# Kernel tuning notes

Hardware: AMD Instinct MI355X
Metric: run time of the kernel (lower is better)

The kernel has to match this reference:

```python
import jax, jax.numpy as jnp
import numpy as np

N_NODES = 50000
N_EDGES = 800000
IN_DIM = 128
HID_DIM = 128
N_CLASSES = 64


def gcn_conv(x, edge_index, W, b):
    """PyG GCNConv: add self-loops, sym deg^-1/2 norm, xW, scatter-add, +bias."""
    n = x.shape[0]
    loop = jnp.arange(n, dtype=edge_index.dtype)
    src = jnp.concatenate([edge_index[0], loop])  # [E+N]
    dst = jnp.concatenate([edge_index[1], loop])  # [E+N]
    ones = jnp.ones(src.shape[0], dtype=x.dtype)
    deg = jax.ops.segment_sum(ones, dst, num_segments=n)  # in-degree incl self-loop
    dinv = jnp.where(deg > 0, jax.lax.rsqrt(deg), jnp.zeros_like(deg))
    norm = dinv[src] * dinv[dst]  # [E+N]
    h = x @ W  # [N, out]
    msg = h[src] * norm[:, None]  # [E+N, out] gather + scale
    out = jax.ops.segment_sum(msg, dst, num_segments=n)  # scatter-add
    return out + b


def setup_inputs() -> dict:
    key = jax.random.key(0)
    k1, k2, k3, k4, k5 = jax.random.split(key, 5)
    x = jax.random.normal(k1, (N_NODES, IN_DIM), dtype=jnp.float32)
    edge_index = jax.random.randint(k2, (2, N_EDGES), 0, N_NODES, dtype=jnp.int64)
    # Glorot-style init for the two GCNConv linear weights; zero biases (PyG default)
    s1 = 1.0 / np.sqrt(IN_DIM)
    s2 = 1.0 / np.sqrt(HID_DIM)
    W1 = jax.random.uniform(k3, (IN_DIM, HID_DIM), jnp.float32, -s1, s1)
    b1 = jnp.zeros((HID_DIM,), jnp.float32)
    W2 = jax.random.uniform(k4, (HID_DIM, N_CLASSES), jnp.float32, -s2, s2)
    b2 = jnp.zeros((N_CLASSES,), jnp.float32)
    return {"x": x, "edge_index": edge_index, "W1": W1, "b1": b1, "W2": W2, "b2": b2}


def reference(x, edge_index, W1, b1, W2, b2):
    h = gcn_conv(x, edge_index, W1, b1)
    h = jax.nn.relu(h)
    out = gcn_conv(h, edge_index, W2, b2)
    return out
```

## Files before the change

### kernel.cpp

```cpp
#include <hip/hip_runtime.h>
#include <hip/hip_bf16.h>
#include <hip/hip_fp16.h>


#define NODES_PER_BLOCK 4
#define CHUNK 4096
#define BCAP 8192

typedef unsigned int uint;
typedef _Float16 f16x8 __attribute__((ext_vector_type(8)));
typedef float f32x4 __attribute__((ext_vector_type(4)));

__device__ __forceinline__ float2 h2f(uint v) {
  __half2 h;
  __builtin_memcpy(&h, &v, 4);
  return __half22float2(h);
}

__device__ __forceinline__ uint f2h(float a, float b) {
  __half2 h = __halves2half2(__float2half_rn(a), __float2half_rn(b));
  uint r;
  __builtin_memcpy(&r, &h, 4);
  return r;
}

__global__ void detect64_k(const int* ei, int* flag) {
  int lane = threadIdx.x & 63;
  unsigned long long m = __ballot(ei[2 * lane + 1] != 0);
  if (threadIdx.x == 0) *flag = (m == 0ULL) ? 1 : 0;
}

__global__ __launch_bounds__(256) void hist_k(const int* __restrict__ ei,
                                              const int* __restrict__ flag,
                                              int* __restrict__ gh,
                                              int E, int nchunk, int nbuck) {
  __shared__ int h[256];
  int c = blockIdx.x;
  for (int i = threadIdx.x; i < 256; i += 256) h[i] = 0;
  __syncthreads();
  int is64 = *flag;
  int base = c * CHUNK;
  int lim = min(CHUNK, E - base);
  for (int i = threadIdx.x; i < lim; i += 256) {
    int e = base + i;
    int d = is64 ? ei[2 * ((size_t)E + e)] : ei[(size_t)E + e];
    atomicAdd(&h[d >> 8], 1);
  }
  __syncthreads();
  for (int k = threadIdx.x; k < nbuck; k += 256) gh[k * nchunk + c] = h[k];
}

__global__ __launch_bounds__(256) void tot_k(const int* __restrict__ gh,
                                             int* __restrict__ totals, int nchunk) {
  __shared__ int sd[256];
  int k = blockIdx.x;
  int s = 0;
  for (int i = threadIdx.x; i < nchunk; i += 256) s += gh[k * nchunk + i];
  sd[threadIdx.x] = s;
  __syncthreads();
  for (int o = 128; o > 0; o >>= 1) {
    if (threadIdx.x < o) sd[threadIdx.x] += sd[threadIdx.x + o];
    __syncthreads();
  }
  if (threadIdx.x == 0) totals[k] = sd[0];
}

__global__ __launch_bounds__(256) void scanrow_k(int* __restrict__ gh,
                                                 const int* __restrict__ totals,
                                                 int* __restrict__ bucketStart,
                                                 int* __restrict__ offsets,
                                                 int nchunk, int nbuck, int N, int E) {
  __shared__ int st[256];
  int k = blockIdx.x;
  int t = threadIdx.x;
  int v = (t < nbuck && t < k) ? totals[t] : 0;
  st[t] = v;
  __syncthreads();
  for (int o = 128; o > 0; o >>= 1) {
    if (t < o) st[t] += st[t + o];
    __syncthreads();
  }
  int bs = st[0];
  if (t == 0) {
    bucketStart[k] = bs;
    if (k == nbuck - 1) { bucketStart[nbuck] = E; offsets[N] = E; }
  }
  __syncthreads();
  int x = (t < nchunk) ? gh[k * nchunk + t] : 0;
  st[t] = x;
  __syncthreads();
  int incl = x;
  for (int o = 1; o < 256; o <<= 1) {
    int add = (t >= o) ? st[t - o] : 0;
    __syncthreads();
    incl += add;
    st[t] = incl;
    __syncthreads();
  }
  if (t < nchunk) gh[k * nchunk + t] = bs + (incl - x);
}

__global__ __launch_bounds__(256) void part_k(const int* __restrict__ ei,
                                              const int* __restrict__ flag,
                                              const int* __restrict__ gh,
                                              int* __restrict__ tmp,
                                              int E, int nchunk, int nbuck) {
  __shared__ int cur[256];
  int c = blockIdx.x;
  for (int i = threadIdx.x; i < nbuck; i += 256) cur[i] = gh[i * nchunk + c];
  __syncthreads();
  int is64 = *flag;
  int base = c * CHUNK;
  int lim = min(CHUNK, E - base);
  for (int i = threadIdx.x; i < lim; i += 256) {
    int e = base + i;
    int s, d;
    if (is64) {
      s = ei[2 * (size_t)e];
      d = ei[2 * ((size_t)E + e)];
    } else {
      s = ei[e];
      d = ei[(size_t)E + e];
    }
    int p = atomicAdd(&cur[d >> 8], 1);
    tmp[p] = s | ((d & 255) << 16);
  }
}

__global__ __launch_bounds__(256) void bucket_k(const int* __restrict__ tmp,
                                                const int* __restrict__ bucketStart,
                                                int* __restrict__ csr_src,
                                                int* __restrict__ offsets,
                                                float* __restrict__ dinv,
                                                int N) {
  __shared__ int ebuf[BCAP];
  __shared__ int cnt[256];
  __shared__ int st[256];
  __shared__ int lofs[256];
  int k = blockIdx.x;
  int b0 = bucketStart[k], b1 = bucketStart[k + 1];
  int sz = b1 - b0;
  int t = threadIdx.x;
  cnt[t] = 0;
  __syncthreads();
  bool inlds = (sz <= BCAP);
  if (inlds) {
    for (int i = t; i < sz; i += 256) {
      int v = tmp[b0 + i];
      ebuf[i] = v;
      atomicAdd(&cnt[v >> 16], 1);
    }
  } else {
    for (int i = t; i < sz; i += 256) atomicAdd(&cnt[tmp[b0 + i] >> 16], 1);
  }
  __syncthreads();
  int x = cnt[t];
  st[t] = x;
  __syncthreads();
  int incl = x;
  for (int o = 1; o < 256; o <<= 1) {
    int add = (t >= o) ? st[t - o] : 0;
    __syncthreads();
    incl += add;
    st[t] = incl;
    __syncthreads();
  }
  lofs[t] = incl - x;
  int node = k * 256 + t;
  if (node < N) {
    offsets[node] = b0 + lofs[t];
    dinv[node] = rsqrtf((float)(x + 1));
  }
  __syncthreads();
  cnt[t] = lofs[t];
  __syncthreads();
  if (inlds) {
    for (int i = t; i < sz; i += 256) {
      int v = ebuf[i];
      int p = atomicAdd(&cnt[v >> 16], 1);
      csr_src[b0 + p] = v & 0xFFFF;
    }
  } else {
    for (int i = t; i < sz; i += 256) {
      int v = tmp[b0 + i];
      int p = atomicAdd(&cnt[v >> 16], 1);
      csr_src[b0 + p] = v & 0xFFFF;
    }
  }
}

__global__ void prep_k(const float* __restrict__ W, _Float16* __restrict__ P,
                       int NC, int total) {
  int idx = blockIdx.x * blockDim.x + threadIdx.x;
  if (idx >= total) return;
  int NF = NC >> 4;
  int j = idx & 7;
  int l = (idx >> 3) & 63;
  int rest = idx >> 9;
  int c = rest % NF;
  int t = rest / NF;
  int k = t * 32 + ((l >> 4) << 3) + j;
  int col = c * 16 + (l & 15);
  P[idx] = (_Float16)W[(size_t)k * NC + col];
}

template <int NC, bool A16>
__global__ __launch_bounds__(256) void mfma_gemm_k(const void* __restrict__ Xv,
                                                   const _Float16* __restrict__ Wp,
                                                   const float* __restrict__ dinv,
                                                   _Float16* __restrict__ H, int M) {
  constexpr int NF = NC / 16;
  int lane = threadIdx.x & 63;
  int w = threadIdx.x >> 6;
  int row0 = blockIdx.x * 64 + w * 16;
  int arow = row0 + (lane & 15);
  bool av = arow < M;
  const uint4* wp = (const uint4*)Wp;

  f32x4 acc[NF];
#pragma unroll
  for (int c = 0; c < NF; ++c) acc[c] = (f32x4){0.f, 0.f, 0.f, 0.f};

#pragma unroll
  for (int t = 0; t < 4; ++t) {
    f16x8 a;
    if constexpr (A16) {
      const _Float16* xr = (const _Float16*)Xv + (size_t)arow * 128 + ((lane >> 4) << 3);
      uint4 araw = av ? *(const uint4*)(xr + t * 32)
                      : make_uint4(0u, 0u, 0u, 0u);
      __builtin_memcpy(&a, &araw, 16);
    } else {
      const float* xr = (const float*)Xv + (size_t)arow * 128 + ((lane >> 4) << 3);
      float4 lo = av ? *(const float4*)(xr + t * 32)
                     : make_float4(0.f, 0.f, 0.f, 0.f);
      float4 hi = av ? *(const float4*)(xr + t * 32 + 4)
                     : make_float4(0.f, 0.f, 0.f, 0.f);
      a[0] = (_Float16)lo.x; a[1] = (_Float16)lo.y;
      a[2] = (_Float16)lo.z; a[3] = (_Float16)lo.w;
      a[4] = (_Float16)hi.x; a[5] = (_Float16)hi.y;
      a[6] = (_Float16)hi.z; a[7] = (_Float16)hi.w;
    }
#pragma unroll
    for (int c = 0; c < NF; ++c) {
      uint4 braw = wp[(t * NF + c) * 64 + lane];
      f16x8 b;
      __builtin_memcpy(&b, &braw, 16);
      acc[c] = __builtin_amdgcn_mfma_f32_16x16x32_f16(a, b, acc[c], 0, 0, 0);
    }
  }

  int rbase = row0 + ((lane >> 4) << 2);
#pragma unroll
  for (int r = 0; r < 4; ++r) {
    int row = rbase + r;
    if (row < M) {
      float di = dinv[row];
#pragma unroll
      for (int c = 0; c < NF; ++c)
        H[(size_t)row * NC + c * 16 + (lane & 15)] = (_Float16)(di * acc[c][r]);
    }
  }
}

__global__ __launch_bounds__(256) void agg1_k(const uint* __restrict__ hp,
                                              const float* __restrict__ dinv,
                                              const int* __restrict__ offsets,
                                              const int* __restrict__ csr_src,
                                              const float* __restrict__ b,
                                              uint* __restrict__ y, int n) {
  int wave = threadIdx.x >> 6;
  int lane = threadIdx.x & 63;
  int node = blockIdx.x * NODES_PER_BLOCK + wave;
  if (node >= n) return;
  int beg = offsets[node], end = offsets[node + 1];
  int deg = end - beg;
  float2 self = h2f(hp[(size_t)node * 64 + lane]);
  float ax = self.x, ay = self.y;
  int sv = 0;
  if (lane < deg) sv = csr_src[beg + lane];
  int lim = deg < 64 ? deg : 64;
  int e = 0;
  for (; e + 8 <= lim; e += 8) {
    int s0 = __shfl(sv, e + 0), s1 = __shfl(sv, e + 1);
    int s2 = __shfl(sv, e + 2), s3 = __shfl(sv, e + 3);
    int s4 = __shfl(sv, e + 4), s5 = __shfl(sv, e + 5);
    int s6 = __shfl(sv, e + 6), s7 = __shfl(sv, e + 7);
    uint u0 = hp[(size_t)s0 * 64 + lane];
    uint u1 = hp[(size_t)s1 * 64 + lane];
    uint u2 = hp[(size_t)s2 * 64 + lane];
    uint u3 = hp[(size_t)s3 * 64 + lane];
    uint u4 = hp[(size_t)s4 * 64 + lane];
    uint u5 = hp[(size_t)s5 * 64 + lane];
    uint u6 = hp[(size_t)s6 * 64 + lane];
    uint u7 = hp[(size_t)s7 * 64 + lane];
    float2 v0 = h2f(u0), v1 = h2f(u1), v2 = h2f(u2), v3 = h2f(u3);
    float2 v4 = h2f(u4), v5 = h2f(u5), v6 = h2f(u6), v7 = h2f(u7);
    ax += ((v0.x + v1.x) + (v2.x + v3.x)) + ((v4.x + v5.x) + (v6.x + v7.x));
    ay += ((v0.y + v1.y) + (v2.y + v3.y)) + ((v4.y + v5.y) + (v6.y + v7.y));
  }
  for (; e < lim; ++e) {
    int s = __shfl(sv, e);
    float2 v = h2f(hp[(size_t)s * 64 + lane]);
    ax += v.x;
    ay += v.y;
  }
  for (int ee = beg + 64; ee < end; ++ee) {
    float2 v = h2f(hp[(size_t)csr_src[ee] * 64 + lane]);
    ax += v.x;
    ay += v.y;
  }
  float di = dinv[node];
  float2 bb = ((const float2*)b)[lane];
  float ox = fmaxf(fmaf(di, ax, bb.x), 0.0f);
  float oy = fmaxf(fmaf(di, ay, bb.y), 0.0f);
  y[(size_t)node * 64 + lane] = f2h(ox, oy);
}

__global__ __launch_bounds__(256) void agg2_k(const uint* __restrict__ hp,
                                              const float* __restrict__ dinv,
                                              const int* __restrict__ offsets,
                                              const int* __restrict__ csr_src,
                                              const float* __restrict__ b,
                                              float* __restrict__ out, int n) {
  int wv = threadIdx.x >> 6;
  int lane = threadIdx.x & 63;
  int half = lane >> 5;
  int fl = lane & 31;
  int node = blockIdx.x * 8 + wv * 2 + half;
  if (node >= n) return;
  int beg = offsets[node], end = offsets[node + 1];
  int deg = end - beg;
  float2 self = h2f(hp[(size_t)node * 32 + fl]);
  float ax = self.x, ay = self.y;
  int sv = 0;
  if (fl < deg) sv = csr_src[beg + fl];
  int lim = deg < 32 ? deg : 32;
  int e = 0;
  for (; e + 8 <= lim; e += 8) {
    int s0 = __shfl(sv, e + 0, 32), s1 = __shfl(sv, e + 1, 32);
    int s2 = __shfl(sv, e + 2, 32), s3 = __shfl(sv, e + 3, 32);
    int s4 = __shfl(sv, e + 4, 32), s5 = __shfl(sv, e + 5, 32);
    int s6 = __shfl(sv, e + 6, 32), s7 = __shfl(sv, e + 7, 32);
    uint u0 = hp[(size_t)s0 * 32 + fl];
    uint u1 = hp[(size_t)s1 * 32 + fl];
    uint u2 = hp[(size_t)s2 * 32 + fl];
    uint u3 = hp[(size_t)s3 * 32 + fl];
    uint u4 = hp[(size_t)s4 * 32 + fl];
    uint u5 = hp[(size_t)s5 * 32 + fl];
    uint u6 = hp[(size_t)s6 * 32 + fl];
    uint u7 = hp[(size_t)s7 * 32 + fl];
    float2 v0 = h2f(u0), v1 = h2f(u1), v2 = h2f(u2), v3 = h2f(u3);
    float2 v4 = h2f(u4), v5 = h2f(u5), v6 = h2f(u6), v7 = h2f(u7);
    ax += ((v0.x + v1.x) + (v2.x + v3.x)) + ((v4.x + v5.x) + (v6.x + v7.x));
    ay += ((v0.y + v1.y) + (v2.y + v3.y)) + ((v4.y + v5.y) + (v6.y + v7.y));
  }
  for (; e < lim; ++e) {
    int s = __shfl(sv, e, 32);
    float2 v = h2f(hp[(size_t)s * 32 + fl]);
    ax += v.x;
    ay += v.y;
  }
  for (int ee = beg + 32; ee < end; ++ee) {
    float2 v = h2f(hp[(size_t)csr_src[ee] * 32 + fl]);
    ax += v.x;
    ay += v.y;
  }
  float di = dinv[node];
  float2 bb = ((const float2*)b)[fl];
  float2 o;
  o.x = fmaf(di, ax, bb.x);
  o.y = fmaf(di, ay, bb.y);
  ((float2*)out)[(size_t)node * 32 + fl] = o;
}

extern "C" void kernel_launch(void* const* d_in, const int* in_sizes, int n_in,
                              void* d_out, int out_size, void* d_ws, size_t ws_size,
                              hipStream_t stream) {
  const float* x  = (const float*)d_in[0];
  const int*   ei = (const int*)d_in[1];
  const float* W1 = (const float*)d_in[2];
  const float* b1 = (const float*)d_in[3];
  const float* W2 = (const float*)d_in[4];
  const float* b2 = (const float*)d_in[5];
  float* out = (float*)d_out;

  const int N = in_sizes[0] / 128;
  const int E = in_sizes[1] / 2;
  const int NBUCK = (N + 255) >> 8;
  const int NCHUNK = (E + CHUNK - 1) / CHUNK;

  char* w = (char*)d_ws;
  size_t off = 0;
  auto alloc = [&](size_t bytes) -> void* {
    void* p = w + off;
    off = (off + bytes + 511) & ~(size_t)511;
    return p;
  };
  int*       gh      = (int*)alloc((size_t)NBUCK * NCHUNK * 4);
  int*       totals  = (int*)alloc((size_t)NBUCK * 4);
  int*       bstart  = (int*)alloc((size_t)(NBUCK + 1) * 4);
  int*       flag    = (int*)alloc(64);
  int*       tmp     = (int*)alloc((size_t)E * 4);
  int*       offsets = (int*)alloc((size_t)(N + 1) * 4);
  float*     dinv    = (float*)alloc((size_t)N * 4);
  int*       csr_src = (int*)alloc((size_t)E * 4);
  _Float16*  pW1     = (_Float16*)alloc(16384 * 2);
  _Float16*  pW2     = (_Float16*)alloc(8192 * 2);
  _Float16*  h1      = (_Float16*)alloc((size_t)N * 128 * 2);
  _Float16*  y       = (_Float16*)alloc((size_t)N * 128 * 2);
  _Float16*  h2      = (_Float16*)alloc((size_t)N * 64 * 2);

  const int GB  = (N + 63) / 64;
  const int AB  = (N + NODES_PER_BLOCK - 1) / NODES_PER_BLOCK;
  const int AB2 = (N + 7) / 8;

  detect64_k<<<1, 64, 0, stream>>>(ei, flag);
  hist_k<<<NCHUNK, 256, 0, stream>>>(ei, flag, gh, E, NCHUNK, NBUCK);
  tot_k<<<NBUCK, 256, 0, stream>>>(gh, totals, NCHUNK);
  scanrow_k<<<NBUCK, 256, 0, stream>>>(gh, totals, bstart, offsets, NCHUNK, NBUCK, N, E);
  part_k<<<NCHUNK, 256, 0, stream>>>(ei, flag, gh, tmp, E, NCHUNK, NBUCK);
  bucket_k<<<NBUCK, 256, 0, stream>>>(tmp, bstart, csr_src, offsets, dinv, N);

  prep_k<<<64, 256, 0, stream>>>(W1, pW1, 128, 16384);
  prep_k<<<32, 256, 0, stream>>>(W2, pW2, 64, 8192);

  mfma_gemm_k<128, false><<<GB, 256, 0, stream>>>(x, pW1, dinv, h1, N);
  agg1_k<<<AB, 256, 0, stream>>>((const uint*)h1, dinv, offsets, csr_src, b1,
                                 (uint*)y, N);
  mfma_gemm_k<64, true><<<GB, 256, 0, stream>>>(y, pW2, dinv, h2, N);
  agg2_k<<<AB2, 256, 0, stream>>>((const uint*)h2, dinv, offsets, csr_src, b2, out, N);
}
```

Measured before the change: 118.0 us.

## Fuse CSR-build launches, shrink buckets, and widen agg1 to half-wave per node

Folds the int64 detection into each block and merges the weight-packing kernels into the histogram launch. It also drops the separate totals kernel by summing prefix chunks inside scanrow, which cuts kernel launches from twelve to eight. Buckets shrink from 256 to 128 nodes, giving more bucket_k blocks and a smaller LDS buffer. agg1 now processes two nodes per wave with 8-byte loads per lane, so each gather uses more of the wave. The tradeoff is redundant prefix summation in scanrow and a lower 32-edge shuffle limit before the slow per-edge fallback path in agg1.

After: 141.1 us. 19.6% more time.

```diff
diff --git a/kernel.cpp b/kernel.cpp
--- a/kernel.cpp
+++ b/kernel.cpp
@@ -3,9 +3,10 @@
 #include <hip/hip_fp16.h>
 
 
-#define NODES_PER_BLOCK 4
 #define CHUNK 4096
-#define BCAP 8192
+#define BSHIFT 7
+#define BSIZE 128
+#define BCAP 4096
 
 typedef unsigned int uint;
 typedef _Float16 f16x8 __attribute__((ext_vector_type(8)));
@@ -24,57 +25,68 @@
   return r;
 }
 
-__global__ void detect64_k(const int* ei, int* flag) {
-  int lane = threadIdx.x & 63;
-  unsigned long long m = __ballot(ei[2 * lane + 1] != 0);
-  if (threadIdx.x == 0) *flag = (m == 0ULL) ? 1 : 0;
-}
-
-__global__ __launch_bounds__(256) void hist_k(const int* __restrict__ ei,
-                                              const int* __restrict__ flag,
-                                              int* __restrict__ gh,
-                                              int E, int nchunk, int nbuck) {
-  __shared__ int h[256];
+__device__ __forceinline__ int block_is64(const int* ei, int* s_is64) {
+  if (threadIdx.x < 64) {
+    unsigned long long m = __ballot(ei[2 * threadIdx.x + 1] != 0);
+    if (threadIdx.x == 0) *s_is64 = (m == 0ULL) ? 1 : 0;
+  }
+  __syncthreads();
+  return *s_is64;
+}
+
+__global__ __launch_bounds__(256) void hist_prep_k(const int* __restrict__ ei,
+                                                   int* __restrict__ gh,
+                                                   const float* __restrict__ W1,
+                                                   const float* __restrict__ W2,
+                                                   _Float16* __restrict__ P,
+                                                   int E, int nchunk, int nbuck) {
+  if (blockIdx.x >= nchunk) {
+    int li = (blockIdx.x - nchunk) * 256 + threadIdx.x;
+    if (li >= 24576) return;
+    const float* W;
+    _Float16* dst;
+    int NC, idx;
+    if (li < 16384) { W = W1; dst = P;         NC = 128; idx = li; }
+    else            { W = W2; dst = P + 16384; NC = 64;  idx = li - 16384; }
+    int NF = NC >> 4;
+    int j = idx & 7;
+    int l = (idx >> 3) & 63;
+    int rest = idx >> 9;
+    int c = rest % NF;
+    int t = rest / NF;
+    int k = t * 32 + ((l >> 4) << 3) + j;
+    int col = c * 16 + (l & 15);
+    dst[idx] = (_Float16)W[(size_t)k * NC + col];
+    return;
+  }
+  __shared__ int h[512];
+  __shared__ int s_is64;
   int c = blockIdx.x;
-  for (int i = threadIdx.x; i < 256; i += 256) h[i] = 0;
-  __syncthreads();
-  int is64 = *flag;
+  for (int i = threadIdx.x; i < 512; i += 256) h[i] = 0;
+  int is64 = block_is64(ei, &s_is64);
   int base = c * CHUNK;
   int lim = min(CHUNK, E - base);
   for (int i = threadIdx.x; i < lim; i += 256) {
     int e = base + i;
     int d = is64 ? ei[2 * ((size_t)E + e)] : ei[(size_t)E + e];
-    atomicAdd(&h[d >> 8], 1);
+    atomicAdd(&h[d >> BSHIFT], 1);
   }
   __syncthreads();
   for (int k = threadIdx.x; k < nbuck; k += 256) gh[k * nchunk + c] = h[k];
 }
 
-__global__ __launch_bounds__(256) void tot_k(const int* __restrict__ gh,
-                                             int* __restrict__ totals, int nchunk) {
-  __shared__ int sd[256];
-  int k = blockIdx.x;
-  int s = 0;
-  for (int i = threadIdx.x; i < nchunk; i += 256) s += gh[k * nchunk + i];
-  sd[threadIdx.x] = s;
-  __syncthreads();
-  for (int o = 128; o > 0; o >>= 1) {
-    if (threadIdx.x < o) sd[threadIdx.x] += sd[threadIdx.x + o];
-    __syncthreads();
-  }
-  if (threadIdx.x == 0) totals[k] = sd[0];
-}
-
-__global__ __launch_bounds__(256) void scanrow_k(int* __restrict__ gh,
-                                                 const int* __restrict__ totals,
+__global__ __launch_bounds__(256) void scanrow_k(const int* __restrict__ gh,
+                                                 int* __restrict__ gbase,
                                                  int* __restrict__ bucketStart,
                                                  int* __restrict__ offsets,
                                                  int nchunk, int nbuck, int N, int E) {
   __shared__ int st[256];
   int k = blockIdx.x;
   int t = threadIdx.x;
-  int v = (t < nbuck && t < k) ? totals[t] : 0;
-  st[t] = v;
+  int tot = k * nchunk;
+  int partial = 0;
+  for (int i = t; i < tot; i += 256) partial += gh[i];
+  st[t] = partial;
   __syncthreads();
   for (int o = 128; o > 0; o >>= 1) {
     if (t < o) st[t] += st[t + o];
@@ -97,19 +109,18 @@
     st[t] = incl;
     __syncthreads();
   }
-  if (t < nchunk) gh[k * nchunk + t] = bs + (incl - x);
+  if (t < nchunk) gbase[k * nchunk + t] = bs + (incl - x);
 }
 
 __global__ __launch_bounds__(256) void part_k(const int* __restrict__ ei,
-                                              const int* __restrict__ flag,
-                                              const int* __restrict__ gh,
+                                              const int* __restrict__ gbase,
                                               int* __restrict__ tmp,
                                               int E, int nchunk, int nbuck) {
-  __shared__ int cur[256];
+  __shared__ int cur[512];
+  __shared__ int s_is64;
   int c = blockIdx.x;
-  for (int i = threadIdx.x; i < nbuck; i += 256) cur[i] = gh[i * nchunk + c];
-  __syncthreads();
-  int is64 = *flag;
+  for (int i = threadIdx.x; i < nbuck; i += 256) cur[i] = gbase[i * nchunk + c];
+  int is64 = block_is64(ei, &s_is64);
   int base = c * CHUNK;
   int lim = min(CHUNK, E - base);
   for (int i = threadIdx.x; i < lim; i += 256) {
@@ -122,8 +133,8 @@
       s = ei[e];
       d = ei[(size_t)E + e];
     }
-    int p = atomicAdd(&cur[d >> 8], 1);
-    tmp[p] = s | ((d & 255) << 16);
+    int p = atomicAdd(&cur[d >> BSHIFT], 1);
+    tmp[p] = s | ((d & (BSIZE - 1)) << 16);
   }
 }
 
@@ -134,14 +145,14 @@
                                                 float* __restrict__ dinv,
                                                 int N) {
   __shared__ int ebuf[BCAP];
-  __shared__ int cnt[256];
+  __shared__ int cnt[BSIZE];
   __shared__ int st[256];
-  __shared__ int lofs[256];
+  __shared__ int lofs[BSIZE];
   int k = blockIdx.x;
   int b0 = bucketStart[k], b1 = bucketStart[k + 1];
   int sz = b1 - b0;
   int t = threadIdx.x;
-  cnt[t] = 0;
+  if (t < BSIZE) cnt[t] = 0;
   __syncthreads();
   bool inlds = (sz <= BCAP);
   if (inlds) {
@@ -154,7 +165,7 @@
     for (int i = t; i < sz; i += 256) atomicAdd(&cnt[tmp[b0 + i] >> 16], 1);
   }
   __syncthreads();
-  int x = cnt[t];
+  int x = (t < BSIZE) ? cnt[t] : 0;
   st[t] = x;
   __syncthreads();
   int incl = x;
@@ -165,14 +176,16 @@
     st[t] = incl;
     __syncthreads();
   }
-  lofs[t] = incl - x;
-  int node = k * 256 + t;
-  if (node < N) {
-    offsets[node] = b0 + lofs[t];
-    dinv[node] = rsqrtf((float)(x + 1));
-  }
-  __syncthreads();
-  cnt[t] = lofs[t];
+  int node = (k << BSHIFT) + t;
+  if (t < BSIZE) {
+    lofs[t] = incl - x;
+    if (node < N) {
+      offsets[node] = b0 + lofs[t];
+      dinv[node] = rsqrtf((float)(x + 1));
+    }
+  }
+  __syncthreads();
+  if (t < BSIZE) cnt[t] = lofs[t];
   __syncthreads();
   if (inlds) {
     for (int i = t; i < sz; i += 256) {
@@ -187,21 +200,6 @@
       csr_src[b0 + p] = v & 0xFFFF;
     }
   }
-}
-
-__global__ void prep_k(const float* __restrict__ W, _Float16* __restrict__ P,
-                       int NC, int total) {
-  int idx = blockIdx.x * blockDim.x + threadIdx.x;
-  if (idx >= total) return;
-  int NF = NC >> 4;
-  int j = idx & 7;
-  int l = (idx >> 3) & 63;
-  int rest = idx >> 9;
-  int c = rest % NF;
-  int t = rest / NF;
-  int k = t * 32 + ((l >> 4) << 3) + j;
-  int col = c * 16 + (l & 15);
-  P[idx] = (_Float16)W[(size_t)k * NC + col];
 }
 
 template <int NC, bool A16>
@@ -226,15 +224,12 @@
     f16x8 a;
     if constexpr (A16) {
       const _Float16* xr = (const _Float16*)Xv + (size_t)arow * 128 + ((lane >> 4) << 3);
-      uint4 araw = av ? *(const uint4*)(xr + t * 32)
-                      : make_uint4(0u, 0u, 0u, 0u);
+      uint4 araw = av ? *(const uint4*)(xr + t * 32) : make_uint4(0u, 0u, 0u, 0u);
       __builtin_memcpy(&a, &araw, 16);
     } else {
       const float* xr = (const float*)Xv + (size_t)arow * 128 + ((lane >> 4) << 3);
-      float4 lo = av ? *(const float4*)(xr + t * 32)
-                     : make_float4(0.f, 0.f, 0.f, 0.f);
-      float4 hi = av ? *(const float4*)(xr + t * 32 + 4)
-                     : make_float4(0.f, 0.f, 0.f, 0.f);
+      float4 lo = av ? *(const float4*)(xr + t * 32) : make_float4(0.f, 0.f, 0.f, 0.f);
+      float4 hi = av ? *(const float4*)(xr + t * 32 + 4) : make_float4(0.f, 0.f, 0.f, 0.f);
       a[0] = (_Float16)lo.x; a[1] = (_Float16)lo.y;
       a[2] = (_Float16)lo.z; a[3] = (_Float16)lo.w;
       a[4] = (_Float16)hi.x; a[5] = (_Float16)hi.y;
@@ -262,58 +257,70 @@
   }
 }
 
-__global__ __launch_bounds__(256) void agg1_k(const uint* __restrict__ hp,
+__global__ __launch_bounds__(256) void agg1_k(const uint2* __restrict__ hp,
                                               const float* __restrict__ dinv,
                                               const int* __restrict__ offsets,
                                               const int* __restrict__ csr_src,
                                               const float* __restrict__ b,
-                                              uint* __restrict__ y, int n) {
-  int wave = threadIdx.x >> 6;
+                                              uint2* __restrict__ y, int n) {
+  int wv = threadIdx.x >> 6;
   int lane = threadIdx.x & 63;
-  int node = blockIdx.x * NODES_PER_BLOCK + wave;
+  int half = lane >> 5;
+  int fl = lane & 31;
+  int node = blockIdx.x * 8 + wv * 2 + half;
   if (node >= n) return;
   int beg = offsets[node], end = offsets[node + 1];
   int deg = end - beg;
-  float2 self = h2f(hp[(size_t)node * 64 + lane]);
-  float ax = self.x, ay = self.y;
+  uint2 su = hp[(size_t)node * 32 + fl];
+  float2 sl = h2f(su.x), sh = h2f(su.y);
+  float a0 = sl.x, a1 = sl.y, a2 = sh.x, a3 = sh.y;
   int sv = 0;
-  if (lane < deg) sv = csr_src[beg + lane];
-  int lim = deg < 64 ? deg : 64;
+  if (fl < deg) sv = csr_src[beg + fl];
+  int lim = deg < 32 ? deg : 32;
   int e = 0;
   for (; e + 8 <= lim; e += 8) {
-    int s0 = __shfl(sv, e + 0), s1 = __shfl(sv, e + 1);
-    int s2 = __shfl(sv, e + 2), s3 = __shfl(sv, e + 3);
-    int s4 = __shfl(sv, e + 4), s5 = __shfl(sv, e + 5);
-    int s6 = __shfl(sv, e + 6), s7 = __shfl(sv, e + 7);
-    uint u0 = hp[(size_t)s0 * 64 + lane];
-    uint u1 = hp[(size_t)s1 * 64 + lane];
-    uint u2 = hp[(size_t)s2 * 64 + lane];
-    uint u3 = hp[(size_t)s3 * 64 + lane];
-    uint u4 = hp[(size_t)s4 * 64 + lane];
-    uint u5 = hp[(size_t)s5 * 64 + lane];
-    uint u6 = hp[(size_t)s6 * 64 + lane];
-    uint u7 = hp[(size_t)s7 * 64 + lane];
-    float2 v0 = h2f(u0), v1 = h2f(u1), v2 = h2f(u2), v3 = h2f(u3);
-    float2 v4 = h2f(u4), v5 = h2f(u5), v6 = h2f(u6), v7 = h2f(u7);
-    ax += ((v0.x + v1.x) + (v2.x + v3.x)) + ((v4.x + v5.x) + (v6.x + v7.x));
-    ay += ((v0.y + v1.y) + (v2.y + v3.y)) + ((v4.y + v5.y) + (v6.y + v7.y));
+    int sA = __shfl(sv, e + 0, 32), sB = __shfl(sv, e + 1, 32);
+    int sC = __shfl(sv, e + 2, 32), sD = __shfl(sv, e + 3, 32);
+    int sE = __shfl(sv, e + 4, 32), sF = __shfl(sv, e + 5, 32);
+    int sG = __shfl(sv, e + 6, 32), sH = __shfl(sv, e + 7, 32);
+    uint2 uA = hp[(size_t)sA * 32 + fl];
+    uint2 uB = hp[(size_t)sB * 32 + fl];
+    uint2 uC = hp[(size_t)sC * 32 + fl];
+    uint2 uD = hp[(size_t)sD * 32 + fl];
+    uint2 uE = hp[(size_t)sE * 32 + fl];
+    uint2 uF = hp[(size_t)sF * 32 + fl];
+    uint2 uG = hp[(size_t)sG * 32 + fl];
+    uint2 uH = hp[(size_t)sH * 32 + fl];
+    float2 lA = h2f(uA.x), hA = h2f(uA.y), lB = h2f(uB.x), hB = h2f(uB.y);
+    float2 lC = h2f(uC.x), hC = h2f(uC.y), lD = h2f(uD.x), hD = h2f(uD.y);
+    float2 lE = h2f(uE.x), hE = h2f(uE.y), lF = h2f(uF.x), hF = h2f(uF.y);
+    float2 lG = h2f(uG.x), hG = h2f(uG.y), lH = h2f(uH.x), hH = h2f(uH.y);
+    a0 += ((lA.x + lB.x) + (lC.x + lD.x)) + ((lE.x + lF.x) + (lG.x + lH.x));
+    a1 += ((lA.y + lB.y) + (lC.y + lD.y)) + ((lE.y + lF.y) + (lG.y + lH.y));
+    a2 += ((hA.x + hB.x) + (hC.x + hD.x)) + ((hE.x + hF.x) + (hG.x + hH.x));
+    a3 += ((hA.y + hB.y) + (hC.y + hD.y)) + ((hE.y + hF.y) + (hG.y + hH.y));
   }
   for (; e < lim; ++e) {
-    int s = __shfl(sv, e);
-    float2 v = h2f(hp[(size_t)s * 64 + lane]);
-    ax += v.x;
-    ay += v.y;
-  }
-  for (int ee = beg + 64; ee < end; ++ee) {
-    float2 v = h2f(hp[(size_t)csr_src[ee] * 64 + lane]);
-    ax += v.x;
-    ay += v.y;
+    int s = __shfl(sv, e, 32);
+    uint2 u = hp[(size_t)s * 32 + fl];
+    float2 l = h2f(u.x), h = h2f(u.y);
+    a0 += l.x; a1 += l.y; a2 += h.x; a3 += h.y;
+  }
+  for (int ee = beg + 32; ee < end; ++ee) {
+    uint2 u = hp[(size_t)csr_src[ee] * 32 + fl];
+    float2 l = h2f(u.x), h = h2f(u.y);
+    a0 += l.x; a1 += l.y; a2 += h.x; a3 += h.y;
   }
   float di = dinv[node];
-  float2 bb = ((const float2*)b)[lane];
-  float ox = fmaxf(fmaf(di, ax, bb.x), 0.0f);
-  float oy = fmaxf(fmaf(di, ay, bb.y), 0.0f);
-  y[(size_t)node * 64 + lane] = f2h(ox, oy);
+  float4 bb = *(const float4*)(b + 4 * fl);
+  float o0 = fmaxf(fmaf(di, a0, bb.x), 0.f);
+  float o1 = fmaxf(fmaf(di, a1, bb.y), 0.f);
+  float o2 = fmaxf(fmaf(di, a2, bb.z), 0.f);
+  float o3 = fmaxf(fmaf(di, a3, bb.w), 0.f);
+  uint2 o;
+  o.x = f2h(o0, o1);
+  o.y = f2h(o2, o3);
+  y[(size_t)node * 32 + fl] = o;
 }
 
 __global__ __launch_bounds__(256) void agg2_k(const uint* __restrict__ hp,
@@ -386,7 +393,7 @@
 
   const int N = in_sizes[0] / 128;
   const int E = in_sizes[1] / 2;
-  const int NBUCK = (N + 255) >> 8;
+  const int NBUCK = (N + BSIZE - 1) >> BSHIFT;
   const int NCHUNK = (E + CHUNK - 1) / CHUNK;
 
   char* w = (char*)d_ws;
@@ -397,36 +404,28 @@
     return p;
   };
   int*       gh      = (int*)alloc((size_t)NBUCK * NCHUNK * 4);
-  int*       totals  = (int*)alloc((size_t)NBUCK * 4);
+  int*       gbase   = (int*)alloc((size_t)NBUCK * NCHUNK * 4);
   int*       bstart  = (int*)alloc((size_t)(NBUCK + 1) * 4);
-  int*       flag    = (int*)alloc(64);
   int*       tmp     = (int*)alloc((size_t)E * 4);
   int*       offsets = (int*)alloc((size_t)(N + 1) * 4);
   float*     dinv    = (float*)alloc((size_t)N * 4);
   int*       csr_src = (int*)alloc((size_t)E * 4);
-  _Float16*  pW1     = (_Float16*)alloc(16384 * 2);
-  _Float16*  pW2     = (_Float16*)alloc(8192 * 2);
+  _Float16*  pW      = (_Float16*)alloc(24576 * 2);
   _Float16*  h1      = (_Float16*)alloc((size_t)N * 128 * 2);
   _Float16*  y       = (_Float16*)alloc((size_t)N * 128 * 2);
   _Float16*  h2      = (_Float16*)alloc((size_t)N * 64 * 2);
 
   const int GB  = (N + 63) / 64;
-  const int AB  = (N + NODES_PER_BLOCK - 1) / NODES_PER_BLOCK;
-  const int AB2 = (N + 7) / 8;
-
-  detect64_k<<<1, 64, 0, stream>>>(ei, flag);
-  hist_k<<<NCHUNK, 256, 0, stream>>>(ei, flag, gh, E, NCHUNK, NBUCK);
-  tot_k<<<NBUCK, 256, 0, stream>>>(gh, totals, NCHUNK);
-  scanrow_k<<<NBUCK, 256, 0, stream>>>(gh, totals, bstart, offsets, NCHUNK, NBUCK, N, E);
-  part_k<<<NCHUNK, 256, 0, stream>>>(ei, flag, gh, tmp, E, NCHUNK, NBUCK);
+  const int AB  = (N + 7) / 8;
+
+  hist_prep_k<<<NCHUNK + 96, 256, 0, stream>>>(ei, gh, W1, W2, pW, E, NCHUNK, NBUCK);
+  scanrow_k<<<NBUCK, 256, 0, stream>>>(gh, gbase, bstart, offsets, NCHUNK, NBUCK, N, E);
+  part_k<<<NCHUNK, 256, 0, stream>>>(ei, gbase, tmp, E, NCHUNK, NBUCK);
   bucket_k<<<NBUCK, 256, 0, stream>>>(tmp, bstart, csr_src, offsets, dinv, N);
 
-  prep_k<<<64, 256, 0, stream>>>(W1, pW1, 128, 16384);
-  prep_k<<<32, 256, 0, stream>>>(W2, pW2, 64, 8192);
-
-  mfma_gemm_k<128, false><<<GB, 256, 0, stream>>>(x, pW1, dinv, h1, N);
-  agg1_k<<<AB, 256, 0, stream>>>((const uint*)h1, dinv, offsets, csr_src, b1,
-                                 (uint*)y, N);
-  mfma_gemm_k<64, true><<<GB, 256, 0, stream>>>(y, pW2, dinv, h2, N);
-  agg2_k<<<AB2, 256, 0, stream>>>((const uint*)h2, dinv, offsets, csr_src, b2, out, N);
-}
+  mfma_gemm_k<128, false><<<GB, 256, 0, stream>>>(x, pW, dinv, h1, N);
+  agg1_k<<<AB, 256, 0, stream>>>((const uint2*)h1, dinv, offsets, csr_src, b1,
+                                 (uint2*)y, N);
+  mfma_gemm_k<64, true><<<GB, 256, 0, stream>>>(y, pW + 16384, dinv, h2, N);
+  agg2_k<<<AB, 256, 0, stream>>>((const uint*)h2, dinv, offsets, csr_src, b2, out, N);
+}
```
